# Kernel optimization log

Measured on AMD Instinct MI355X. Metric: run time of the kernel, lower is better.

Reference implementation:

```python
import jax, jax.numpy as jnp
import numpy as np

NR = 512      # num robots
NT = 1024     # num tasks
E = 500000    # num edges
D = 64        # robot_dim == task_dim (forced by torch.cat dim=0)
ED = 32       # edge_dim
GH = 128      # gnn_hidden
MH = 128      # mlp_hidden
SLOPE = 0.1   # LeakyReLU negative slope


def lrelu(x):
    return jnp.where(x >= 0, x, SLOPE * x)


def _linear(key, out_d, in_d):
    k1, k2 = jax.random.split(key)
    s = 1.0 / np.sqrt(in_d)
    W = jax.random.uniform(k1, (out_d, in_d), minval=-s, maxval=s, dtype=jnp.float32)
    b = jax.random.uniform(k2, (out_d,), minval=-s, maxval=s, dtype=jnp.float32)
    return W, b


def setup_inputs() -> dict:
    key = jax.random.key(0)
    ks = jax.random.split(key, 12)
    x_robot = jax.random.normal(ks[0], (NR, D), dtype=jnp.float32)
    x_task = jax.random.normal(ks[1], (NT, D), dtype=jnp.float32)
    edge_attr = jax.random.normal(ks[2], (E, ED), dtype=jnp.float32)
    src = jax.random.randint(ks[3], (E,), 0, NR)
    tgt = jax.random.randint(ks[4], (E,), 0, NT)
    edge_index = jnp.stack([src, tgt], axis=0).astype(jnp.int64)
    We1, be1 = _linear(ks[5], GH, 2 * D + ED)   # f_theta_e layer 1
    We2, be2 = _linear(ks[6], GH, GH)            # f_theta_e layer 2
    Wv1, bv1 = _linear(ks[7], GH, D + GH)        # f_theta_v layer 1
    Wv2, bv2 = _linear(ks[8], GH, GH)            # f_theta_v layer 2
    Wm1, bm1 = _linear(ks[9], MH, GH + D)        # task selector layer 1
    Wm2, bm2 = _linear(ks[10], 1, MH)            # task selector layer 2
    return {
        'x_robot': x_robot, 'x_task': x_task, 'edge_index': edge_index,
        'edge_attr': edge_attr,
        'We1': We1, 'be1': be1, 'We2': We2, 'be2': be2,
        'Wv1': Wv1, 'bv1': bv1, 'Wv2': Wv2, 'bv2': bv2,
        'Wm1': Wm1, 'bm1': bm1, 'Wm2': Wm2, 'bm2': bm2,
    }


def reference(x_robot, x_task, edge_index, edge_attr,
              We1, be1, We2, be2, Wv1, bv1, Wv2, bv2, Wm1, bm1, Wm2, bm2):
    n_robot = x_robot.shape[0]
    x = jnp.concatenate([x_robot, x_task], axis=0)          # [NR+NT, D]
    src = edge_index[0]                                      # robot indices
    tgt = edge_index[1] + n_robot                            # shifted task indices
    # PyG default flow='source_to_target': x_i = x[target], x_j = x[source],
    # messages are scatter-added at target slots (the task slots here).
    msg_in = jnp.concatenate([x[tgt], x[src], edge_attr], axis=1)  # [E, 2D+ED]
    m = lrelu(msg_in @ We1.T + be1) @ We2.T + be2            # [E, GH]
    agg = jax.ops.segment_sum(m, tgt, num_segments=n_robot + x_task.shape[0])
    robot_msgs = agg[:n_robot]                               # all zeros (faithful to source)
    upd_in = jnp.concatenate([robot_msgs, x_robot], axis=1)  # [NR, GH+D]
    h = lrelu(upd_in @ Wv1.T + bv1) @ Wv2.T + bv2            # [NR, GH]
    # Pairwise MLP on concat([h_i, task_j]) without materializing the concat:
    # split Wm1 columns into the robot-hidden and task parts.
    hr = h @ Wm1[:, :GH].T                                   # [NR, MH]
    ht = x_task @ Wm1[:, GH:].T                              # [NT, MH]
    hid = lrelu(hr[:, None, :] + ht[None, :, :] + bm1)       # [NR, NT, MH]
    scores = jnp.einsum('nmh,h->nm', hid, Wm2[0]) + bm2[0]   # [NR, NT]
    return jax.nn.softmax(scores, axis=1)
```

## Files before the change

kernel.cpp:

```cpp
#include <hip/hip_runtime.h>

#define NRB 512
#define NTK 1024
#define DD  64
#define GHH 128



__global__ __launch_bounds__(256) void prep_kernel(
    const float* __restrict__ xr, const float* __restrict__ xt,
    const float* __restrict__ Wv1, const float* __restrict__ bv1,
    const float* __restrict__ Wv2, const float* __restrict__ bv2,
    const float* __restrict__ Wm1, const float* __restrict__ bm1,
    const float* __restrict__ Wm2, const float* __restrict__ bm2,
    float* __restrict__ HR, float* __restrict__ HTBt4,
    float* __restrict__ av, float* __restrict__ cv, float* __restrict__ wbv)
{
    const int t = threadIdx.x;
    const int b = blockIdx.x;
    const int i = t & 127;
    const int g = t >> 7;

    __shared__ float lds_w[128 * 132];
    __shared__ float xs[8 * 64];
    __shared__ float sA[4 * 132];
    __shared__ float sB[4 * 132];
    __shared__ float sT[8 * 132];
    __shared__ float sR[8 * 132];

    float4* Lw = reinterpret_cast<float4*>(lds_w);

    if (b < 128) {
        const int r0 = b * 4;
        xs[t] = xr[r0 * DD + t];

        {
            const float4* W = reinterpret_cast<const float4*>(Wv1);
            #pragma unroll
            for (int j = 0; j < 8; ++j) {
                const int e = t + 256 * j;
                const int row = e >> 4, c4 = e & 15;
                Lw[row * 33 + c4] = W[row * 48 + 32 + c4];
            }
        }
        __syncthreads();

        {
            float a0 = bv1[i], a1 = a0;
            const float4* w4 = Lw + i * 33;
            const float4* x0 = reinterpret_cast<const float4*>(xs + (2*g)*64);
            const float4* x1 = reinterpret_cast<const float4*>(xs + (2*g+1)*64);
            #pragma unroll
            for (int k = 0; k < 16; ++k) {
                const float4 w = w4[k];
                const float4 p = x0[k];
                const float4 q = x1[k];
                a0 = fmaf(w.x, p.x, a0); a1 = fmaf(w.x, q.x, a1);
                a0 = fmaf(w.y, p.y, a0); a1 = fmaf(w.y, q.y, a1);
                a0 = fmaf(w.z, p.z, a0); a1 = fmaf(w.z, q.z, a1);
                a0 = fmaf(w.w, p.w, a0); a1 = fmaf(w.w, q.w, a1);
            }
            sA[(2*g)*132 + i]   = (a0 >= 0.f) ? a0 : 0.1f * a0;
            sA[(2*g+1)*132 + i] = (a1 >= 0.f) ? a1 : 0.1f * a1;
        }
        __syncthreads();

        {
            const float4* W = reinterpret_cast<const float4*>(Wv2);
            #pragma unroll
            for (int j = 0; j < 16; ++j) {
                const int e = t + 256 * j;
                const int row = e >> 5, c4 = e & 31;
                Lw[row * 33 + c4] = W[row * 32 + c4];
            }
        }
        __syncthreads();

        {
            float a0 = bv2[i], a1 = a0;
            const float4* w4 = Lw + i * 33;
            const float4* h0 = reinterpret_cast<const float4*>(sA + (2*g)*132);
            const float4* h1 = reinterpret_cast<const float4*>(sA + (2*g+1)*132);
            #pragma unroll 8
            for (int k = 0; k < 32; ++k) {
                const float4 w = w4[k];
                const float4 p = h0[k];
                const float4 q = h1[k];
                a0 = fmaf(w.x, p.x, a0); a1 = fmaf(w.x, q.x, a1);
                a0 = fmaf(w.y, p.y, a0); a1 = fmaf(w.y, q.y, a1);
                a0 = fmaf(w.z, p.z, a0); a1 = fmaf(w.z, q.z, a1);
                a0 = fmaf(w.w, p.w, a0); a1 = fmaf(w.w, q.w, a1);
            }
            sB[(2*g)*132 + i]   = a0;
            sB[(2*g+1)*132 + i] = a1;
        }
        __syncthreads();

        {
            const float4* W = reinterpret_cast<const float4*>(Wm1);
            #pragma unroll
            for (int j = 0; j < 16; ++j) {
                const int e = t + 256 * j;
                const int row = e >> 5, c4 = e & 31;
                Lw[row * 33 + c4] = W[row * 48 + c4];
            }
        }
        __syncthreads();

        {
            const float wm2 = Wm2[i];
            float a0 = 0.f, a1 = 0.f;
            const float4* w4 = Lw + i * 33;
            const float4* h0 = reinterpret_cast<const float4*>(sB + (2*g)*132);
            const float4* h1 = reinterpret_cast<const float4*>(sB + (2*g+1)*132);
            #pragma unroll 8
            for (int k = 0; k < 32; ++k) {
                const float4 w = w4[k];
                const float4 p = h0[k];
                const float4 q = h1[k];
                a0 = fmaf(w.x, p.x, a0); a1 = fmaf(w.x, q.x, a1);
                a0 = fmaf(w.y, p.y, a0); a1 = fmaf(w.y, q.y, a1);
                a0 = fmaf(w.z, p.z, a0); a1 = fmaf(w.z, q.z, a1);
                a0 = fmaf(w.w, p.w, a0); a1 = fmaf(w.w, q.w, a1);
            }
            HR[(r0 + 2*g) * GHH + i]     = a0;
            HR[(r0 + 2*g + 1) * GHH + i] = a1;
            sR[(2*g)*132 + i]   = wm2 * a0;
            sR[(2*g+1)*132 + i] = wm2 * a1;
        }
        __syncthreads();

        {
            const int row = t >> 6, c = t & 63;
            float s = sR[row*132 + c] + sR[row*132 + c + 64];
            #pragma unroll
            for (int off = 32; off >= 1; off >>= 1)
                s += __shfl_xor(s, off, 64);
            if (c == 0) av[r0 + row] = 0.55f * s;
        }
    } else {
        const int t0 = (b - 128) * 8;
        xs[t]       = xt[t0 * DD + t];
        xs[256 + t] = xt[t0 * DD + 256 + t];

        {
            const float4* W = reinterpret_cast<const float4*>(Wm1);
            #pragma unroll
            for (int j = 0; j < 8; ++j) {
                const int e = t + 256 * j;
                const int row = e >> 4, c4 = e & 15;
                Lw[row * 33 + c4] = W[row * 48 + 32 + c4];
            }
        }
        __syncthreads();

        {
            const float bb  = bm1[i];
            const float wm2 = Wm2[i];
            float a0 = bb, a1 = bb, a2 = bb, a3 = bb;
            const float4* w4 = Lw + i * 33;
            const float4* x0 = reinterpret_cast<const float4*>(xs + (4*g)*64);
            const float4* x1 = reinterpret_cast<const float4*>(xs + (4*g+1)*64);
            const float4* x2 = reinterpret_cast<const float4*>(xs + (4*g+2)*64);
            const float4* x3 = reinterpret_cast<const float4*>(xs + (4*g+3)*64);
            #pragma unroll
            for (int k = 0; k < 16; ++k) {
                const float4 w = w4[k];
                const float4 p0 = x0[k], p1 = x1[k], p2 = x2[k], p3 = x3[k];
                a0 = fmaf(w.x, p0.x, a0); a1 = fmaf(w.x, p1.x, a1);
                a2 = fmaf(w.x, p2.x, a2); a3 = fmaf(w.x, p3.x, a3);
                a0 = fmaf(w.y, p0.y, a0); a1 = fmaf(w.y, p1.y, a1);
                a2 = fmaf(w.y, p2.y, a2); a3 = fmaf(w.y, p3.y, a3);
                a0 = fmaf(w.z, p0.z, a0); a1 = fmaf(w.z, p1.z, a1);
                a2 = fmaf(w.z, p2.z, a2); a3 = fmaf(w.z, p3.z, a3);
                a0 = fmaf(w.w, p0.w, a0); a1 = fmaf(w.w, p1.w, a1);
                a2 = fmaf(w.w, p2.w, a2); a3 = fmaf(w.w, p3.w, a3);
            }
            sT[(4*g)*132 + i]   = a0;  sR[(4*g)*132 + i]   = wm2 * a0;
            sT[(4*g+1)*132 + i] = a1;  sR[(4*g+1)*132 + i] = wm2 * a1;
            sT[(4*g+2)*132 + i] = a2;  sR[(4*g+2)*132 + i] = wm2 * a2;
            sT[(4*g+3)*132 + i] = a3;  sR[(4*g+3)*132 + i] = wm2 * a3;
        }
        __syncthreads();

        {
            const int h4 = t >> 3, tk = t & 7;
            float4 v;
            v.x = sT[tk*132 + 4*h4 + 0];
            v.y = sT[tk*132 + 4*h4 + 1];
            v.z = sT[tk*132 + 4*h4 + 2];
            v.w = sT[tk*132 + 4*h4 + 3];
            reinterpret_cast<float4*>(HTBt4)[h4 * NTK + t0 + tk] = v;
        }

        {
            const int row = t >> 5, c = t & 31;
            float s = sR[row*132 + c]      + sR[row*132 + c + 32]
                    + sR[row*132 + c + 64] + sR[row*132 + c + 96];
            #pragma unroll
            for (int off = 16; off >= 1; off >>= 1)
                s += __shfl_xor(s, off, 32);
            if (c == 0) cv[t0 + row] = 0.55f * s + bm2[0];
        }
        if (b == 128 && t < GHH) wbv[t] = 0.45f * Wm2[t];
    }
}

__global__ __launch_bounds__(1024) void score_softmax_kernel(
    const float* __restrict__ HR, const float* __restrict__ HTBt4,
    const float* __restrict__ av, const float* __restrict__ cv,
    const float* __restrict__ wbv, float* __restrict__ out)
{
    const int b   = blockIdx.x;
    const int tid = threadIdx.x;
    const int n0  = b * 2;

    const float4* tb  = reinterpret_cast<const float4*>(HTBt4) + tid;
    const float4* hrA = reinterpret_cast<const float4*>(HR + n0 * GHH);
    const float4* hrB = reinterpret_cast<const float4*>(HR + (n0 + 1) * GHH);
    const float4* wb4 = reinterpret_cast<const float4*>(wbv);

    float acc0 = 0.f, acc1 = 0.f;

    #pragma unroll 4
    for (int h4 = 0; h4 < 32; ++h4) {
        const float4 v  = tb[h4 << 10];
        const float4 w  = wb4[h4];
        const float4 r0 = hrA[h4];
        const float4 r1 = hrB[h4];
        acc0 = fmaf(w.x, fabsf(r0.x + v.x), acc0);
        acc1 = fmaf(w.x, fabsf(r1.x + v.x), acc1);
        acc0 = fmaf(w.y, fabsf(r0.y + v.y), acc0);
        acc1 = fmaf(w.y, fabsf(r1.y + v.y), acc1);
        acc0 = fmaf(w.z, fabsf(r0.z + v.z), acc0);
        acc1 = fmaf(w.z, fabsf(r1.z + v.z), acc1);
        acc0 = fmaf(w.w, fabsf(r0.w + v.w), acc0);
        acc1 = fmaf(w.w, fabsf(r1.w + v.w), acc1);
    }

    const float cm = cv[tid];
    float sc[2];
    sc[0] = acc0 + av[n0]     + cm;
    sc[1] = acc1 + av[n0 + 1] + cm;

    __shared__ float rmax[2][16], rsum[2][16];
    const int wid = tid >> 6, lane = tid & 63;

    #pragma unroll
    for (int n = 0; n < 2; ++n) {
        float mx = sc[n];
        #pragma unroll
        for (int off = 32; off >= 1; off >>= 1)
            mx = fmaxf(mx, __shfl_xor(mx, off, 64));
        if (lane == 0) rmax[n][wid] = mx;
    }
    __syncthreads();

    float ex[2];
    #pragma unroll
    for (int n = 0; n < 2; ++n) {
        float mx = rmax[n][0];
        #pragma unroll
        for (int k = 1; k < 16; ++k) mx = fmaxf(mx, rmax[n][k]);
        float e = expf(sc[n] - mx);
        ex[n] = e;
        float s = e;
        #pragma unroll
        for (int off = 32; off >= 1; off >>= 1) s += __shfl_xor(s, off, 64);
        if (lane == 0) rsum[n][wid] = s;
    }
    __syncthreads();

    #pragma unroll
    for (int n = 0; n < 2; ++n) {
        float s = rsum[n][0];
        #pragma unroll
        for (int k = 1; k < 16; ++k) s += rsum[n][k];
        out[(n0 + n) * NTK + tid] = ex[n] * (1.0f / s);
    }
}

extern "C" void kernel_launch(void* const* d_in, const int* in_sizes, int n_in,
                              void* d_out, int out_size, void* d_ws, size_t ws_size,
                              hipStream_t stream)
{
    const float* xr  = (const float*)d_in[0];
    const float* xt  = (const float*)d_in[1];
    const float* Wv1 = (const float*)d_in[8];
    const float* bv1 = (const float*)d_in[9];
    const float* Wv2 = (const float*)d_in[10];
    const float* bv2 = (const float*)d_in[11];
    const float* Wm1 = (const float*)d_in[12];
    const float* bm1 = (const float*)d_in[13];
    const float* Wm2 = (const float*)d_in[14];
    const float* bm2 = (const float*)d_in[15];

    float* ws    = (float*)d_ws;
    float* HR    = ws;
    float* HTBt4 = ws + 65536;
    float* av    = ws + 196608;
    float* cv    = ws + 197120;
    float* wbv   = ws + 198144;
    float* out   = (float*)d_out;

    hipLaunchKernelGGL(prep_kernel, dim3(256), dim3(256), 0, stream,
                       xr, xt, Wv1, bv1, Wv2, bv2, Wm1, bm1, Wm2, bm2,
                       HR, HTBt4, av, cv, wbv);
    hipLaunchKernelGGL(score_softmax_kernel, dim3(256), dim3(1024), 0, stream,
                       HR, HTBt4, av, cv, wbv, out);
}
```

Measured before the change: 22.53 us.

## Fuse robot-side MLP into score/softmax kernel, keep task prep separate

Moves the robot hidden-state chain (Wv1, Wv2, Wm1 robot part, and the av term) out of the prep kernel and into the score/softmax kernel, where each block computes its two robots' HR rows in shared memory. The prep kernel now handles only task-side work, with half as many blocks. This removes the HR/av/wbv global round trip. In exchange, each 1024-thread score block reloads three 128x128 weight matrices into LDS, runs three serial matvecs on only 256 active threads, and needs about 70KB of LDS, which may limit occupancy.

```diff
diff --git a/kernel.cpp b/kernel.cpp
--- a/kernel.cpp
+++ b/kernel.cpp
@@ -7,14 +7,11 @@
 
 
 
-__global__ __launch_bounds__(256) void prep_kernel(
-    const float* __restrict__ xr, const float* __restrict__ xt,
-    const float* __restrict__ Wv1, const float* __restrict__ bv1,
-    const float* __restrict__ Wv2, const float* __restrict__ bv2,
+__global__ __launch_bounds__(256) void task_prep_kernel(
+    const float* __restrict__ xt,
     const float* __restrict__ Wm1, const float* __restrict__ bm1,
     const float* __restrict__ Wm2, const float* __restrict__ bm2,
-    float* __restrict__ HR, float* __restrict__ HTBt4,
-    float* __restrict__ av, float* __restrict__ cv, float* __restrict__ wbv)
+    float* __restrict__ HTBt4, float* __restrict__ cv)
 {
     const int t = threadIdx.x;
     const int b = blockIdx.x;
@@ -23,202 +20,206 @@
 
     __shared__ float lds_w[128 * 132];
     __shared__ float xs[8 * 64];
-    __shared__ float sA[4 * 132];
-    __shared__ float sB[4 * 132];
     __shared__ float sT[8 * 132];
     __shared__ float sR[8 * 132];
 
     float4* Lw = reinterpret_cast<float4*>(lds_w);
 
-    if (b < 128) {
-        const int r0 = b * 4;
-        xs[t] = xr[r0 * DD + t];
-
-        {
-            const float4* W = reinterpret_cast<const float4*>(Wv1);
-            #pragma unroll
-            for (int j = 0; j < 8; ++j) {
-                const int e = t + 256 * j;
-                const int row = e >> 4, c4 = e & 15;
-                Lw[row * 33 + c4] = W[row * 48 + 32 + c4];
-            }
-        }
-        __syncthreads();
-
-        {
-            float a0 = bv1[i], a1 = a0;
-            const float4* w4 = Lw + i * 33;
-            const float4* x0 = reinterpret_cast<const float4*>(xs + (2*g)*64);
-            const float4* x1 = reinterpret_cast<const float4*>(xs + (2*g+1)*64);
-            #pragma unroll
-            for (int k = 0; k < 16; ++k) {
-                const float4 w = w4[k];
-                const float4 p = x0[k];
-                const float4 q = x1[k];
-                a0 = fmaf(w.x, p.x, a0); a1 = fmaf(w.x, q.x, a1);
-                a0 = fmaf(w.y, p.y, a0); a1 = fmaf(w.y, q.y, a1);
-                a0 = fmaf(w.z, p.z, a0); a1 = fmaf(w.z, q.z, a1);
-                a0 = fmaf(w.w, p.w, a0); a1 = fmaf(w.w, q.w, a1);
-            }
-            sA[(2*g)*132 + i]   = (a0 >= 0.f) ? a0 : 0.1f * a0;
-            sA[(2*g+1)*132 + i] = (a1 >= 0.f) ? a1 : 0.1f * a1;
-        }
-        __syncthreads();
-
-        {
-            const float4* W = reinterpret_cast<const float4*>(Wv2);
-            #pragma unroll
-            for (int j = 0; j < 16; ++j) {
-                const int e = t + 256 * j;
-                const int row = e >> 5, c4 = e & 31;
-                Lw[row * 33 + c4] = W[row * 32 + c4];
-            }
-        }
-        __syncthreads();
-
-        {
-            float a0 = bv2[i], a1 = a0;
-            const float4* w4 = Lw + i * 33;
-            const float4* h0 = reinterpret_cast<const float4*>(sA + (2*g)*132);
-            const float4* h1 = reinterpret_cast<const float4*>(sA + (2*g+1)*132);
-            #pragma unroll 8
-            for (int k = 0; k < 32; ++k) {
-                const float4 w = w4[k];
-                const float4 p = h0[k];
-                const float4 q = h1[k];
-                a0 = fmaf(w.x, p.x, a0); a1 = fmaf(w.x, q.x, a1);
-                a0 = fmaf(w.y, p.y, a0); a1 = fmaf(w.y, q.y, a1);
-                a0 = fmaf(w.z, p.z, a0); a1 = fmaf(w.z, q.z, a1);
-                a0 = fmaf(w.w, p.w, a0); a1 = fmaf(w.w, q.w, a1);
-            }
-            sB[(2*g)*132 + i]   = a0;
-            sB[(2*g+1)*132 + i] = a1;
-        }
-        __syncthreads();
-
-        {
-            const float4* W = reinterpret_cast<const float4*>(Wm1);
-            #pragma unroll
-            for (int j = 0; j < 16; ++j) {
-                const int e = t + 256 * j;
-                const int row = e >> 5, c4 = e & 31;
-                Lw[row * 33 + c4] = W[row * 48 + c4];
-            }
-        }
-        __syncthreads();
-
-        {
-            const float wm2 = Wm2[i];
-            float a0 = 0.f, a1 = 0.f;
-            const float4* w4 = Lw + i * 33;
-            const float4* h0 = reinterpret_cast<const float4*>(sB + (2*g)*132);
-            const float4* h1 = reinterpret_cast<const float4*>(sB + (2*g+1)*132);
-            #pragma unroll 8
-            for (int k = 0; k < 32; ++k) {
-                const float4 w = w4[k];
-                const float4 p = h0[k];
-                const float4 q = h1[k];
-                a0 = fmaf(w.x, p.x, a0); a1 = fmaf(w.x, q.x, a1);
-                a0 = fmaf(w.y, p.y, a0); a1 = fmaf(w.y, q.y, a1);
-                a0 = fmaf(w.z, p.z, a0); a1 = fmaf(w.z, q.z, a1);
-                a0 = fmaf(w.w, p.w, a0); a1 = fmaf(w.w, q.w, a1);
-            }
-            HR[(r0 + 2*g) * GHH + i]     = a0;
-            HR[(r0 + 2*g + 1) * GHH + i] = a1;
-            sR[(2*g)*132 + i]   = wm2 * a0;
-            sR[(2*g+1)*132 + i] = wm2 * a1;
-        }
-        __syncthreads();
-
-        {
-            const int row = t >> 6, c = t & 63;
-            float s = sR[row*132 + c] + sR[row*132 + c + 64];
-            #pragma unroll
-            for (int off = 32; off >= 1; off >>= 1)
-                s += __shfl_xor(s, off, 64);
-            if (c == 0) av[r0 + row] = 0.55f * s;
-        }
-    } else {
-        const int t0 = (b - 128) * 8;
-        xs[t]       = xt[t0 * DD + t];
-        xs[256 + t] = xt[t0 * DD + 256 + t];
-
-        {
-            const float4* W = reinterpret_cast<const float4*>(Wm1);
-            #pragma unroll
-            for (int j = 0; j < 8; ++j) {
-                const int e = t + 256 * j;
-                const int row = e >> 4, c4 = e & 15;
-                Lw[row * 33 + c4] = W[row * 48 + 32 + c4];
-            }
-        }
-        __syncthreads();
-
-        {
-            const float bb  = bm1[i];
-            const float wm2 = Wm2[i];
-            float a0 = bb, a1 = bb, a2 = bb, a3 = bb;
-            const float4* w4 = Lw + i * 33;
-            const float4* x0 = reinterpret_cast<const float4*>(xs + (4*g)*64);
-            const float4* x1 = reinterpret_cast<const float4*>(xs + (4*g+1)*64);
-            const float4* x2 = reinterpret_cast<const float4*>(xs + (4*g+2)*64);
-            const float4* x3 = reinterpret_cast<const float4*>(xs + (4*g+3)*64);
-            #pragma unroll
-            for (int k = 0; k < 16; ++k) {
-                const float4 w = w4[k];
-                const float4 p0 = x0[k], p1 = x1[k], p2 = x2[k], p3 = x3[k];
-                a0 = fmaf(w.x, p0.x, a0); a1 = fmaf(w.x, p1.x, a1);
-                a2 = fmaf(w.x, p2.x, a2); a3 = fmaf(w.x, p3.x, a3);
-                a0 = fmaf(w.y, p0.y, a0); a1 = fmaf(w.y, p1.y, a1);
-                a2 = fmaf(w.y, p2.y, a2); a3 = fmaf(w.y, p3.y, a3);
-                a0 = fmaf(w.z, p0.z, a0); a1 = fmaf(w.z, p1.z, a1);
-                a2 = fmaf(w.z, p2.z, a2); a3 = fmaf(w.z, p3.z, a3);
-                a0 = fmaf(w.w, p0.w, a0); a1 = fmaf(w.w, p1.w, a1);
-                a2 = fmaf(w.w, p2.w, a2); a3 = fmaf(w.w, p3.w, a3);
-            }
-            sT[(4*g)*132 + i]   = a0;  sR[(4*g)*132 + i]   = wm2 * a0;
-            sT[(4*g+1)*132 + i] = a1;  sR[(4*g+1)*132 + i] = wm2 * a1;
-            sT[(4*g+2)*132 + i] = a2;  sR[(4*g+2)*132 + i] = wm2 * a2;
-            sT[(4*g+3)*132 + i] = a3;  sR[(4*g+3)*132 + i] = wm2 * a3;
-        }
-        __syncthreads();
-
-        {
-            const int h4 = t >> 3, tk = t & 7;
-            float4 v;
-            v.x = sT[tk*132 + 4*h4 + 0];
-            v.y = sT[tk*132 + 4*h4 + 1];
-            v.z = sT[tk*132 + 4*h4 + 2];
-            v.w = sT[tk*132 + 4*h4 + 3];
-            reinterpret_cast<float4*>(HTBt4)[h4 * NTK + t0 + tk] = v;
-        }
-
-        {
-            const int row = t >> 5, c = t & 31;
-            float s = sR[row*132 + c]      + sR[row*132 + c + 32]
-                    + sR[row*132 + c + 64] + sR[row*132 + c + 96];
-            #pragma unroll
-            for (int off = 16; off >= 1; off >>= 1)
-                s += __shfl_xor(s, off, 32);
-            if (c == 0) cv[t0 + row] = 0.55f * s + bm2[0];
-        }
-        if (b == 128 && t < GHH) wbv[t] = 0.45f * Wm2[t];
+    const int t0 = b * 8;
+    xs[t]       = xt[t0 * DD + t];
+    xs[256 + t] = xt[t0 * DD + 256 + t];
+
+    {
+        const float4* W = reinterpret_cast<const float4*>(Wm1);
+        #pragma unroll
+        for (int j = 0; j < 8; ++j) {
+            const int e = t + 256 * j;
+            const int row = e >> 4, c4 = e & 15;
+            Lw[row * 33 + c4] = W[row * 48 + 32 + c4];
+        }
+    }
+    __syncthreads();
+
+    {
+        const float bb  = bm1[i];
+        const float wm2 = Wm2[i];
+        float a0 = bb, a1 = bb, a2 = bb, a3 = bb;
+        const float4* w4 = Lw + i * 33;
+        const float4* x0 = reinterpret_cast<const float4*>(xs + (4*g)*64);
+        const float4* x1 = reinterpret_cast<const float4*>(xs + (4*g+1)*64);
+        const float4* x2 = reinterpret_cast<const float4*>(xs + (4*g+2)*64);
+        const float4* x3 = reinterpret_cast<const float4*>(xs + (4*g+3)*64);
+        #pragma unroll
+        for (int k = 0; k < 16; ++k) {
+            const float4 w = w4[k];
+            const float4 p0 = x0[k], p1 = x1[k], p2 = x2[k], p3 = x3[k];
+            a0 = fmaf(w.x, p0.x, a0); a1 = fmaf(w.x, p1.x, a1);
+            a2 = fmaf(w.x, p2.x, a2); a3 = fmaf(w.x, p3.x, a3);
+            a0 = fmaf(w.y, p0.y, a0); a1 = fmaf(w.y, p1.y, a1);
+            a2 = fmaf(w.y, p2.y, a2); a3 = fmaf(w.y, p3.y, a3);
+            a0 = fmaf(w.z, p0.z, a0); a1 = fmaf(w.z, p1.z, a1);
+            a2 = fmaf(w.z, p2.z, a2); a3 = fmaf(w.z, p3.z, a3);
+            a0 = fmaf(w.w, p0.w, a0); a1 = fmaf(w.w, p1.w, a1);
+            a2 = fmaf(w.w, p2.w, a2); a3 = fmaf(w.w, p3.w, a3);
+        }
+        sT[(4*g)*132 + i]   = a0;  sR[(4*g)*132 + i]   = wm2 * a0;
+        sT[(4*g+1)*132 + i] = a1;  sR[(4*g+1)*132 + i] = wm2 * a1;
+        sT[(4*g+2)*132 + i] = a2;  sR[(4*g+2)*132 + i] = wm2 * a2;
+        sT[(4*g+3)*132 + i] = a3;  sR[(4*g+3)*132 + i] = wm2 * a3;
+    }
+    __syncthreads();
+
+    {
+        const int h4 = t >> 3, tk = t & 7;
+        float4 v;
+        v.x = sT[tk*132 + 4*h4 + 0];
+        v.y = sT[tk*132 + 4*h4 + 1];
+        v.z = sT[tk*132 + 4*h4 + 2];
+        v.w = sT[tk*132 + 4*h4 + 3];
+        reinterpret_cast<float4*>(HTBt4)[h4 * NTK + t0 + tk] = v;
+    }
+
+    {
+        const int row = t >> 5, c = t & 31;
+        float s = sR[row*132 + c]      + sR[row*132 + c + 32]
+                + sR[row*132 + c + 64] + sR[row*132 + c + 96];
+        #pragma unroll
+        for (int off = 16; off >= 1; off >>= 1)
+            s += __shfl_xor(s, off, 32);
+        if (c == 0) cv[t0 + row] = 0.55f * s + bm2[0];
     }
 }
 
-__global__ __launch_bounds__(1024) void score_softmax_kernel(
-    const float* __restrict__ HR, const float* __restrict__ HTBt4,
-    const float* __restrict__ av, const float* __restrict__ cv,
-    const float* __restrict__ wbv, float* __restrict__ out)
+__global__ __launch_bounds__(1024) void robot_score_softmax_kernel(
+    const float* __restrict__ xr,
+    const float* __restrict__ Wv1, const float* __restrict__ bv1,
+    const float* __restrict__ Wv2, const float* __restrict__ bv2,
+    const float* __restrict__ Wm1, const float* __restrict__ Wm2,
+    const float* __restrict__ HTBt4, const float* __restrict__ cv,
+    float* __restrict__ out)
 {
     const int b   = blockIdx.x;
     const int tid = threadIdx.x;
     const int n0  = b * 2;
 
+    __shared__ float lds_w[128 * 132];
+    __shared__ float xs[2 * 64];
+    __shared__ float sA[2 * 132];
+    __shared__ float sB[2 * 132];
+    __shared__ float sR[2 * 132];
+    __shared__ float s_hr[2 * 128];
+    __shared__ float s_wb[128];
+    __shared__ float s_av[2];
+
+    float4* Lw = reinterpret_cast<float4*>(lds_w);
+
+    const float cm = cv[tid];
+
+    if (tid < 128) xs[tid] = xr[n0 * DD + tid];
+
+    {
+        const float4* W = reinterpret_cast<const float4*>(Wv1);
+        #pragma unroll
+        for (int j = 0; j < 2; ++j) {
+            const int e = tid + 1024 * j;
+            const int row = e >> 4, c4 = e & 15;
+            Lw[row * 33 + c4] = W[row * 48 + 32 + c4];
+        }
+    }
+    __syncthreads();
+
+    if (tid < 256) {
+        const int i = tid & 127, r = tid >> 7;
+        float acc = bv1[i];
+        const float4* w4 = Lw + i * 33;
+        const float4* x4 = reinterpret_cast<const float4*>(xs + r * 64);
+        #pragma unroll
+        for (int k = 0; k < 16; ++k) {
+            const float4 w = w4[k];
+            const float4 p = x4[k];
+            acc = fmaf(w.x, p.x, acc);
+            acc = fmaf(w.y, p.y, acc);
+            acc = fmaf(w.z, p.z, acc);
+            acc = fmaf(w.w, p.w, acc);
+        }
+        sA[r*132 + i] = (acc >= 0.f) ? acc : 0.1f * acc;
+    }
+    __syncthreads();
+
+    {
+        const float4* W = reinterpret_cast<const float4*>(Wv2);
+        #pragma unroll
+        for (int j = 0; j < 4; ++j) {
+            const int e = tid + 1024 * j;
+            const int row = e >> 5, c4 = e & 31;
+            Lw[row * 33 + c4] = W[row * 32 + c4];
+        }
+    }
+    __syncthreads();
+
+    if (tid < 256) {
+        const int i = tid & 127, r = tid >> 7;
+        float acc = bv2[i];
+        const float4* w4 = Lw + i * 33;
+        const float4* h4 = reinterpret_cast<const float4*>(sA + r * 132);
+        #pragma unroll 8
+        for (int k = 0; k < 32; ++k) {
+            const float4 w = w4[k];
+            const float4 p = h4[k];
+            acc = fmaf(w.x, p.x, acc);
+            acc = fmaf(w.y, p.y, acc);
+            acc = fmaf(w.z, p.z, acc);
+            acc = fmaf(w.w, p.w, acc);
+        }
+        sB[r*132 + i] = acc;
+    }
+    __syncthreads();
+
+    {
+        const float4* W = reinterpret_cast<const float4*>(Wm1);
+        #pragma unroll
+        for (int j = 0; j < 4; ++j) {
+            const int e = tid + 1024 * j;
+            const int row = e >> 5, c4 = e & 31;
+            Lw[row * 33 + c4] = W[row * 48 + c4];
+        }
+        if (tid < 128) s_wb[tid] = 0.45f * Wm2[tid];
+    }
+    __syncthreads();
+
+    if (tid < 256) {
+        const int i = tid & 127, r = tid >> 7;
+        float acc = 0.f;
+        const float4* w4 = Lw + i * 33;
+        const float4* h4 = reinterpret_cast<const float4*>(sB + r * 132);
+        #pragma unroll 8
+        for (int k = 0; k < 32; ++k) {
+            const float4 w = w4[k];
+            const float4 p = h4[k];
+            acc = fmaf(w.x, p.x, acc);
+            acc = fmaf(w.y, p.y, acc);
+            acc = fmaf(w.z, p.z, acc);
+            acc = fmaf(w.w, p.w, acc);
+        }
+        s_hr[r*128 + i] = acc;
+        sR[r*132 + i]   = Wm2[i] * acc;
+    }
+    __syncthreads();
+
+    if (tid < 128) {
+        const int w = tid >> 6, l = tid & 63;
+        float s = sR[w*132 + l] + sR[w*132 + l + 64];
+        #pragma unroll
+        for (int off = 32; off >= 1; off >>= 1)
+            s += __shfl_xor(s, off, 64);
+        if (l == 0) s_av[w] = 0.55f * s;
+    }
+    __syncthreads();
+
     const float4* tb  = reinterpret_cast<const float4*>(HTBt4) + tid;
-    const float4* hrA = reinterpret_cast<const float4*>(HR + n0 * GHH);
-    const float4* hrB = reinterpret_cast<const float4*>(HR + (n0 + 1) * GHH);
-    const float4* wb4 = reinterpret_cast<const float4*>(wbv);
+    const float4* hrA = reinterpret_cast<const float4*>(s_hr);
+    const float4* hrB = reinterpret_cast<const float4*>(s_hr + 128);
+    const float4* wb4 = reinterpret_cast<const float4*>(s_wb);
 
     float acc0 = 0.f, acc1 = 0.f;
 
@@ -238,10 +239,9 @@
         acc1 = fmaf(w.w, fabsf(r1.w + v.w), acc1);
     }
 
-    const float cm = cv[tid];
     float sc[2];
-    sc[0] = acc0 + av[n0]     + cm;
-    sc[1] = acc1 + av[n0 + 1] + cm;
+    sc[0] = acc0 + s_av[0] + cm;
+    sc[1] = acc1 + s_av[1] + cm;
 
     __shared__ float rmax[2][16], rsum[2][16];
     const int wid = tid >> 6, lane = tid & 63;
@@ -296,16 +296,12 @@
     const float* bm2 = (const float*)d_in[15];
 
     float* ws    = (float*)d_ws;
-    float* HR    = ws;
-    float* HTBt4 = ws + 65536;
-    float* av    = ws + 196608;
-    float* cv    = ws + 197120;
-    float* wbv   = ws + 198144;
+    float* HTBt4 = ws;
+    float* cv    = ws + 131072;
     float* out   = (float*)d_out;
 
-    hipLaunchKernelGGL(prep_kernel, dim3(256), dim3(256), 0, stream,
-                       xr, xt, Wv1, bv1, Wv2, bv2, Wm1, bm1, Wm2, bm2,
-                       HR, HTBt4, av, cv, wbv);
-    hipLaunchKernelGGL(score_softmax_kernel, dim3(256), dim3(1024), 0, stream,
-                       HR, HTBt4, av, cv, wbv, out);
+    hipLaunchKernelGGL(task_prep_kernel, dim3(128), dim3(256), 0, stream,
+                       xt, Wm1, bm1, Wm2, bm2, HTBt4, cv);
+    hipLaunchKernelGGL(robot_score_softmax_kernel, dim3(256), dim3(1024), 0, stream,
+                       xr, Wv1, bv1, Wv2, bv2, Wm1, Wm2, HTBt4, cv, out);
 }
```

New measurement: 24.42 us. 1.08x slower.

## Double rows per block in prep and score kernels, staging HR in shared memory

Applied to the files above, without the earlier changes.

The prep kernel now handles 8 robots or 16 tasks per block, halving the grid to 128 blocks, so each staged weight matrix is reused across twice as many rows. The score/softmax kernel processes 4 robot rows per block instead of 2, with the HR rows and the weight vector staged in LDS, so each loaded HTBt4 tile serves four accumulators. Both changes cut redundant global weight loads. In exchange there are fewer blocks than the GPU's CUs, which lowers parallelism and may hurt latency hiding, and registers per thread go up.

```diff
diff --git a/kernel.cpp b/kernel.cpp
--- a/kernel.cpp
+++ b/kernel.cpp
@@ -22,17 +22,20 @@
     const int g = t >> 7;
 
     __shared__ float lds_w[128 * 132];
-    __shared__ float xs[8 * 64];
-    __shared__ float sA[4 * 132];
-    __shared__ float sB[4 * 132];
-    __shared__ float sT[8 * 132];
-    __shared__ float sR[8 * 132];
+    __shared__ float xs[16 * 64];
+    __shared__ float sU[16 * 132];
+    __shared__ float sV[16 * 132];
 
     float4* Lw = reinterpret_cast<float4*>(lds_w);
 
-    if (b < 128) {
-        const int r0 = b * 4;
-        xs[t] = xr[r0 * DD + t];
+    if (b < 64) {
+        const int r0 = b * 8;
+        xs[t]       = xr[r0 * DD + t];
+        xs[256 + t] = xr[r0 * DD + 256 + t];
+
+        float* sA = sU;
+        float* sB = sV;
+        float* sR = sU + 8 * 132;
 
         {
             const float4* W = reinterpret_cast<const float4*>(Wv1);
@@ -46,117 +49,7 @@
         __syncthreads();
 
         {
-            float a0 = bv1[i], a1 = a0;
-            const float4* w4 = Lw + i * 33;
-            const float4* x0 = reinterpret_cast<const float4*>(xs + (2*g)*64);
-            const float4* x1 = reinterpret_cast<const float4*>(xs + (2*g+1)*64);
-            #pragma unroll
-            for (int k = 0; k < 16; ++k) {
-                const float4 w = w4[k];
-                const float4 p = x0[k];
-                const float4 q = x1[k];
-                a0 = fmaf(w.x, p.x, a0); a1 = fmaf(w.x, q.x, a1);
-                a0 = fmaf(w.y, p.y, a0); a1 = fmaf(w.y, q.y, a1);
-                a0 = fmaf(w.z, p.z, a0); a1 = fmaf(w.z, q.z, a1);
-                a0 = fmaf(w.w, p.w, a0); a1 = fmaf(w.w, q.w, a1);
-            }
-            sA[(2*g)*132 + i]   = (a0 >= 0.f) ? a0 : 0.1f * a0;
-            sA[(2*g+1)*132 + i] = (a1 >= 0.f) ? a1 : 0.1f * a1;
-        }
-        __syncthreads();
-
-        {
-            const float4* W = reinterpret_cast<const float4*>(Wv2);
-            #pragma unroll
-            for (int j = 0; j < 16; ++j) {
-                const int e = t + 256 * j;
-                const int row = e >> 5, c4 = e & 31;
-                Lw[row * 33 + c4] = W[row * 32 + c4];
-            }
-        }
-        __syncthreads();
-
-        {
-            float a0 = bv2[i], a1 = a0;
-            const float4* w4 = Lw + i * 33;
-            const float4* h0 = reinterpret_cast<const float4*>(sA + (2*g)*132);
-            const float4* h1 = reinterpret_cast<const float4*>(sA + (2*g+1)*132);
-            #pragma unroll 8
-            for (int k = 0; k < 32; ++k) {
-                const float4 w = w4[k];
-                const float4 p = h0[k];
-                const float4 q = h1[k];
-                a0 = fmaf(w.x, p.x, a0); a1 = fmaf(w.x, q.x, a1);
-                a0 = fmaf(w.y, p.y, a0); a1 = fmaf(w.y, q.y, a1);
-                a0 = fmaf(w.z, p.z, a0); a1 = fmaf(w.z, q.z, a1);
-                a0 = fmaf(w.w, p.w, a0); a1 = fmaf(w.w, q.w, a1);
-            }
-            sB[(2*g)*132 + i]   = a0;
-            sB[(2*g+1)*132 + i] = a1;
-        }
-        __syncthreads();
-
-        {
-            const float4* W = reinterpret_cast<const float4*>(Wm1);
-            #pragma unroll
-            for (int j = 0; j < 16; ++j) {
-                const int e = t + 256 * j;
-                const int row = e >> 5, c4 = e & 31;
-                Lw[row * 33 + c4] = W[row * 48 + c4];
-            }
-        }
-        __syncthreads();
-
-        {
-            const float wm2 = Wm2[i];
-            float a0 = 0.f, a1 = 0.f;
-            const float4* w4 = Lw + i * 33;
-            const float4* h0 = reinterpret_cast<const float4*>(sB + (2*g)*132);
-            const float4* h1 = reinterpret_cast<const float4*>(sB + (2*g+1)*132);
-            #pragma unroll 8
-            for (int k = 0; k < 32; ++k) {
-                const float4 w = w4[k];
-                const float4 p = h0[k];
-                const float4 q = h1[k];
-                a0 = fmaf(w.x, p.x, a0); a1 = fmaf(w.x, q.x, a1);
-                a0 = fmaf(w.y, p.y, a0); a1 = fmaf(w.y, q.y, a1);
-                a0 = fmaf(w.z, p.z, a0); a1 = fmaf(w.z, q.z, a1);
-                a0 = fmaf(w.w, p.w, a0); a1 = fmaf(w.w, q.w, a1);
-            }
-            HR[(r0 + 2*g) * GHH + i]     = a0;
-            HR[(r0 + 2*g + 1) * GHH + i] = a1;
-            sR[(2*g)*132 + i]   = wm2 * a0;
-            sR[(2*g+1)*132 + i] = wm2 * a1;
-        }
-        __syncthreads();
-
-        {
-            const int row = t >> 6, c = t & 63;
-            float s = sR[row*132 + c] + sR[row*132 + c + 64];
-            #pragma unroll
-            for (int off = 32; off >= 1; off >>= 1)
-                s += __shfl_xor(s, off, 64);
-            if (c == 0) av[r0 + row] = 0.55f * s;
-        }
-    } else {
-        const int t0 = (b - 128) * 8;
-        xs[t]       = xt[t0 * DD + t];
-        xs[256 + t] = xt[t0 * DD + 256 + t];
-
-        {
-            const float4* W = reinterpret_cast<const float4*>(Wm1);
-            #pragma unroll
-            for (int j = 0; j < 8; ++j) {
-                const int e = t + 256 * j;
-                const int row = e >> 4, c4 = e & 15;
-                Lw[row * 33 + c4] = W[row * 48 + 32 + c4];
-            }
-        }
-        __syncthreads();
-
-        {
-            const float bb  = bm1[i];
-            const float wm2 = Wm2[i];
+            const float bb = bv1[i];
             float a0 = bb, a1 = bb, a2 = bb, a3 = bb;
             const float4* w4 = Lw + i * 33;
             const float4* x0 = reinterpret_cast<const float4*>(xs + (4*g)*64);
@@ -176,15 +69,183 @@
                 a0 = fmaf(w.w, p0.w, a0); a1 = fmaf(w.w, p1.w, a1);
                 a2 = fmaf(w.w, p2.w, a2); a3 = fmaf(w.w, p3.w, a3);
             }
-            sT[(4*g)*132 + i]   = a0;  sR[(4*g)*132 + i]   = wm2 * a0;
-            sT[(4*g+1)*132 + i] = a1;  sR[(4*g+1)*132 + i] = wm2 * a1;
-            sT[(4*g+2)*132 + i] = a2;  sR[(4*g+2)*132 + i] = wm2 * a2;
-            sT[(4*g+3)*132 + i] = a3;  sR[(4*g+3)*132 + i] = wm2 * a3;
-        }
-        __syncthreads();
-
-        {
-            const int h4 = t >> 3, tk = t & 7;
+            sA[(4*g)*132 + i]   = (a0 >= 0.f) ? a0 : 0.1f * a0;
+            sA[(4*g+1)*132 + i] = (a1 >= 0.f) ? a1 : 0.1f * a1;
+            sA[(4*g+2)*132 + i] = (a2 >= 0.f) ? a2 : 0.1f * a2;
+            sA[(4*g+3)*132 + i] = (a3 >= 0.f) ? a3 : 0.1f * a3;
+        }
+        __syncthreads();
+
+        {
+            const float4* W = reinterpret_cast<const float4*>(Wv2);
+            #pragma unroll
+            for (int j = 0; j < 16; ++j) {
+                const int e = t + 256 * j;
+                const int row = e >> 5, c4 = e & 31;
+                Lw[row * 33 + c4] = W[row * 32 + c4];
+            }
+        }
+        __syncthreads();
+
+        {
+            const float bb = bv2[i];
+            float a0 = bb, a1 = bb, a2 = bb, a3 = bb;
+            const float4* w4 = Lw + i * 33;
+            const float4* h0 = reinterpret_cast<const float4*>(sA + (4*g)*132);
+            const float4* h1 = reinterpret_cast<const float4*>(sA + (4*g+1)*132);
+            const float4* h2 = reinterpret_cast<const float4*>(sA + (4*g+2)*132);
+            const float4* h3 = reinterpret_cast<const float4*>(sA + (4*g+3)*132);
+            #pragma unroll 8
+            for (int k = 0; k < 32; ++k) {
+                const float4 w = w4[k];
+                const float4 p0 = h0[k], p1 = h1[k], p2 = h2[k], p3 = h3[k];
+                a0 = fmaf(w.x, p0.x, a0); a1 = fmaf(w.x, p1.x, a1);
+                a2 = fmaf(w.x, p2.x, a2); a3 = fmaf(w.x, p3.x, a3);
+                a0 = fmaf(w.y, p0.y, a0); a1 = fmaf(w.y, p1.y, a1);
+                a2 = fmaf(w.y, p2.y, a2); a3 = fmaf(w.y, p3.y, a3);
+                a0 = fmaf(w.z, p0.z, a0); a1 = fmaf(w.z, p1.z, a1);
+                a2 = fmaf(w.z, p2.z, a2); a3 = fmaf(w.z, p3.z, a3);
+                a0 = fmaf(w.w, p0.w, a0); a1 = fmaf(w.w, p1.w, a1);
+                a2 = fmaf(w.w, p2.w, a2); a3 = fmaf(w.w, p3.w, a3);
+            }
+            sB[(4*g)*132 + i]   = a0;
+            sB[(4*g+1)*132 + i] = a1;
+            sB[(4*g+2)*132 + i] = a2;
+            sB[(4*g+3)*132 + i] = a3;
+        }
+        __syncthreads();
+
+        {
+            const float4* W = reinterpret_cast<const float4*>(Wm1);
+            #pragma unroll
+            for (int j = 0; j < 16; ++j) {
+                const int e = t + 256 * j;
+                const int row = e >> 5, c4 = e & 31;
+                Lw[row * 33 + c4] = W[row * 48 + c4];
+            }
+        }
+        __syncthreads();
+
+        {
+            const float wm2 = Wm2[i];
+            float a0 = 0.f, a1 = 0.f, a2 = 0.f, a3 = 0.f;
+            const float4* w4 = Lw + i * 33;
+            const float4* h0 = reinterpret_cast<const float4*>(sB + (4*g)*132);
+            const float4* h1 = reinterpret_cast<const float4*>(sB + (4*g+1)*132);
+            const float4* h2 = reinterpret_cast<const float4*>(sB + (4*g+2)*132);
+            const float4* h3 = reinterpret_cast<const float4*>(sB + (4*g+3)*132);
+            #pragma unroll 8
+            for (int k = 0; k < 32; ++k) {
+                const float4 w = w4[k];
+                const float4 p0 = h0[k], p1 = h1[k], p2 = h2[k], p3 = h3[k];
+                a0 = fmaf(w.x, p0.x, a0); a1 = fmaf(w.x, p1.x, a1);
+                a2 = fmaf(w.x, p2.x, a2); a3 = fmaf(w.x, p3.x, a3);
+                a0 = fmaf(w.y, p0.y, a0); a1 = fmaf(w.y, p1.y, a1);
+                a2 = fmaf(w.y, p2.y, a2); a3 = fmaf(w.y, p3.y, a3);
+                a0 = fmaf(w.z, p0.z, a0); a1 = fmaf(w.z, p1.z, a1);
+                a2 = fmaf(w.z, p2.z, a2); a3 = fmaf(w.z, p3.z, a3);
+                a0 = fmaf(w.w, p0.w, a0); a1 = fmaf(w.w, p1.w, a1);
+                a2 = fmaf(w.w, p2.w, a2); a3 = fmaf(w.w, p3.w, a3);
+            }
+            HR[(r0 + 4*g)     * GHH + i] = a0;
+            HR[(r0 + 4*g + 1) * GHH + i] = a1;
+            HR[(r0 + 4*g + 2) * GHH + i] = a2;
+            HR[(r0 + 4*g + 3) * GHH + i] = a3;
+            sR[(4*g)*132 + i]   = wm2 * a0;
+            sR[(4*g+1)*132 + i] = wm2 * a1;
+            sR[(4*g+2)*132 + i] = wm2 * a2;
+            sR[(4*g+3)*132 + i] = wm2 * a3;
+        }
+        __syncthreads();
+
+        {
+            const int row = t >> 5, c = t & 31;
+            float s = sR[row*132 + c]      + sR[row*132 + c + 32]
+                    + sR[row*132 + c + 64] + sR[row*132 + c + 96];
+            #pragma unroll
+            for (int off = 16; off >= 1; off >>= 1)
+                s += __shfl_xor(s, off, 32);
+            if (c == 0) av[r0 + row] = 0.55f * s;
+        }
+    } else {
+        const int t0 = (b - 64) * 16;
+        xs[t]       = xt[t0 * DD + t];
+        xs[256 + t] = xt[t0 * DD + 256 + t];
+        xs[512 + t] = xt[t0 * DD + 512 + t];
+        xs[768 + t] = xt[t0 * DD + 768 + t];
+
+        float* sT = sU;
+        float* sR = sV;
+
+        {
+            const float4* W = reinterpret_cast<const float4*>(Wm1);
+            #pragma unroll
+            for (int j = 0; j < 8; ++j) {
+                const int e = t + 256 * j;
+                const int row = e >> 4, c4 = e & 15;
+                Lw[row * 33 + c4] = W[row * 48 + 32 + c4];
+            }
+        }
+        __syncthreads();
+
+        {
+            const float bb  = bm1[i];
+            const float wm2 = Wm2[i];
+            float a0 = bb, a1 = bb, a2 = bb, a3 = bb;
+            float a4 = bb, a5 = bb, a6 = bb, a7 = bb;
+            const float4* w4 = Lw + i * 33;
+            const float4* x0 = reinterpret_cast<const float4*>(xs + (8*g)*64);
+            const float4* x1 = reinterpret_cast<const float4*>(xs + (8*g+1)*64);
+            const float4* x2 = reinterpret_cast<const float4*>(xs + (8*g+2)*64);
+            const float4* x3 = reinterpret_cast<const float4*>(xs + (8*g+3)*64);
+            const float4* x4 = reinterpret_cast<const float4*>(xs + (8*g+4)*64);
+            const float4* x5 = reinterpret_cast<const float4*>(xs + (8*g+5)*64);
+            const float4* x6 = reinterpret_cast<const float4*>(xs + (8*g+6)*64);
+            const float4* x7 = reinterpret_cast<const float4*>(xs + (8*g+7)*64);
+            #pragma unroll
+            for (int k = 0; k < 16; ++k) {
+                const float4 w = w4[k];
+                float4 p;
+                p = x0[k];
+                a0 = fmaf(w.x, p.x, a0); a0 = fmaf(w.y, p.y, a0);
+                a0 = fmaf(w.z, p.z, a0); a0 = fmaf(w.w, p.w, a0);
+                p = x1[k];
+                a1 = fmaf(w.x, p.x, a1); a1 = fmaf(w.y, p.y, a1);
+                a1 = fmaf(w.z, p.z, a1); a1 = fmaf(w.w, p.w, a1);
+                p = x2[k];
+                a2 = fmaf(w.x, p.x, a2); a2 = fmaf(w.y, p.y, a2);
+                a2 = fmaf(w.z, p.z, a2); a2 = fmaf(w.w, p.w, a2);
+                p = x3[k];
+                a3 = fmaf(w.x, p.x, a3); a3 = fmaf(w.y, p.y, a3);
+                a3 = fmaf(w.z, p.z, a3); a3 = fmaf(w.w, p.w, a3);
+                p = x4[k];
+                a4 = fmaf(w.x, p.x, a4); a4 = fmaf(w.y, p.y, a4);
+                a4 = fmaf(w.z, p.z, a4); a4 = fmaf(w.w, p.w, a4);
+                p = x5[k];
+                a5 = fmaf(w.x, p.x, a5); a5 = fmaf(w.y, p.y, a5);
+                a5 = fmaf(w.z, p.z, a5); a5 = fmaf(w.w, p.w, a5);
+                p = x6[k];
+                a6 = fmaf(w.x, p.x, a6); a6 = fmaf(w.y, p.y, a6);
+                a6 = fmaf(w.z, p.z, a6); a6 = fmaf(w.w, p.w, a6);
+                p = x7[k];
+                a7 = fmaf(w.x, p.x, a7); a7 = fmaf(w.y, p.y, a7);
+                a7 = fmaf(w.z, p.z, a7); a7 = fmaf(w.w, p.w, a7);
+            }
+            sT[(8*g)*132 + i]   = a0;  sR[(8*g)*132 + i]   = wm2 * a0;
+            sT[(8*g+1)*132 + i] = a1;  sR[(8*g+1)*132 + i] = wm2 * a1;
+            sT[(8*g+2)*132 + i] = a2;  sR[(8*g+2)*132 + i] = wm2 * a2;
+            sT[(8*g+3)*132 + i] = a3;  sR[(8*g+3)*132 + i] = wm2 * a3;
+            sT[(8*g+4)*132 + i] = a4;  sR[(8*g+4)*132 + i] = wm2 * a4;
+            sT[(8*g+5)*132 + i] = a5;  sR[(8*g+5)*132 + i] = wm2 * a5;
+            sT[(8*g+6)*132 + i] = a6;  sR[(8*g+6)*132 + i] = wm2 * a6;
+            sT[(8*g+7)*132 + i] = a7;  sR[(8*g+7)*132 + i] = wm2 * a7;
+        }
+        __syncthreads();
+
+        #pragma unroll
+        for (int j = 0; j < 2; ++j) {
+            const int e  = t + 256 * j;
+            const int h4 = e >> 4, tk = e & 15;
             float4 v;
             v.x = sT[tk*132 + 4*h4 + 0];
             v.y = sT[tk*132 + 4*h4 + 1];
@@ -194,15 +255,16 @@
         }
 
         {
-            const int row = t >> 5, c = t & 31;
-            float s = sR[row*132 + c]      + sR[row*132 + c + 32]
-                    + sR[row*132 + c + 64] + sR[row*132 + c + 96];
-            #pragma unroll
-            for (int off = 16; off >= 1; off >>= 1)
-                s += __shfl_xor(s, off, 32);
+            const int row = t >> 4, c = t & 15;
+            float s = 0.f;
+            #pragma unroll
+            for (int j = 0; j < 8; ++j) s += sR[row*132 + c + 16*j];
+            #pragma unroll
+            for (int off = 8; off >= 1; off >>= 1)
+                s += __shfl_xor(s, off, 16);
             if (c == 0) cv[t0 + row] = 0.55f * s + bm2[0];
         }
-        if (b == 128 && t < GHH) wbv[t] = 0.45f * Wm2[t];
+        if (b == 64 && t < GHH) wbv[t] = 0.45f * Wm2[t];
     }
 }
 
@@ -213,41 +275,58 @@
 {
     const int b   = blockIdx.x;
     const int tid = threadIdx.x;
-    const int n0  = b * 2;
+    const int n0  = b * 4;
+
+    __shared__ float s_hr[4 * GHH];
+    __shared__ float s_wb[GHH];
+    if (tid < 512)      s_hr[tid]       = HR[n0 * GHH + tid];
+    else if (tid < 640) s_wb[tid - 512] = wbv[tid - 512];
+    const float cm = cv[tid];
+    __syncthreads();
 
     const float4* tb  = reinterpret_cast<const float4*>(HTBt4) + tid;
-    const float4* hrA = reinterpret_cast<const float4*>(HR + n0 * GHH);
-    const float4* hrB = reinterpret_cast<const float4*>(HR + (n0 + 1) * GHH);
-    const float4* wb4 = reinterpret_cast<const float4*>(wbv);
-
-    float acc0 = 0.f, acc1 = 0.f;
+    const float4* hr4 = reinterpret_cast<const float4*>(s_hr);
+    const float4* wb4 = reinterpret_cast<const float4*>(s_wb);
+
+    float acc0 = 0.f, acc1 = 0.f, acc2 = 0.f, acc3 = 0.f;
 
     #pragma unroll 4
     for (int h4 = 0; h4 < 32; ++h4) {
         const float4 v  = tb[h4 << 10];
         const float4 w  = wb4[h4];
-        const float4 r0 = hrA[h4];
-        const float4 r1 = hrB[h4];
+        const float4 r0 = hr4[h4];
+        const float4 r1 = hr4[32 + h4];
+        const float4 r2 = hr4[64 + h4];
+        const float4 r3 = hr4[96 + h4];
         acc0 = fmaf(w.x, fabsf(r0.x + v.x), acc0);
         acc1 = fmaf(w.x, fabsf(r1.x + v.x), acc1);
+        acc2 = fmaf(w.x, fabsf(r2.x + v.x), acc2);
+        acc3 = fmaf(w.x, fabsf(r3.x + v.x), acc3);
         acc0 = fmaf(w.y, fabsf(r0.y + v.y), acc0);
         acc1 = fmaf(w.y, fabsf(r1.y + v.y), acc1);
+        acc2 = fmaf(w.y, fabsf(r2.y + v.y), acc2);
+        acc3 = fmaf(w.y, fabsf(r3.y + v.y), acc3);
         acc0 = fmaf(w.z, fabsf(r0.z + v.z), acc0);
         acc1 = fmaf(w.z, fabsf(r1.z + v.z), acc1);
+        acc2 = fmaf(w.z, fabsf(r2.z + v.z), acc2);
+        acc3 = fmaf(w.z, fabsf(r3.z + v.z), acc3);
         acc0 = fmaf(w.w, fabsf(r0.w + v.w), acc0);
         acc1 = fmaf(w.w, fabsf(r1.w + v.w), acc1);
-    }
-
-    const float cm = cv[tid];
-    float sc[2];
+        acc2 = fmaf(w.w, fabsf(r2.w + v.w), acc2);
+        acc3 = fmaf(w.w, fabsf(r3.w + v.w), acc3);
+    }
+
+    float sc[4];
     sc[0] = acc0 + av[n0]     + cm;
     sc[1] = acc1 + av[n0 + 1] + cm;
-
-    __shared__ float rmax[2][16], rsum[2][16];
+    sc[2] = acc2 + av[n0 + 2] + cm;
+    sc[3] = acc3 + av[n0 + 3] + cm;
+
+    __shared__ float rmax[4][16], rsum[4][16];
     const int wid = tid >> 6, lane = tid & 63;
 
     #pragma unroll
-    for (int n = 0; n < 2; ++n) {
+    for (int n = 0; n < 4; ++n) {
         float mx = sc[n];
         #pragma unroll
         for (int off = 32; off >= 1; off >>= 1)
@@ -256,9 +335,9 @@
     }
     __syncthreads();
 
-    float ex[2];
+    float ex[4];
     #pragma unroll
-    for (int n = 0; n < 2; ++n) {
+    for (int n = 0; n < 4; ++n) {
         float mx = rmax[n][0];
         #pragma unroll
         for (int k = 1; k < 16; ++k) mx = fmaxf(mx, rmax[n][k]);
@@ -272,7 +351,7 @@
     __syncthreads();
 
     #pragma unroll
-    for (int n = 0; n < 2; ++n) {
+    for (int n = 0; n < 4; ++n) {
         float s = rsum[n][0];
         #pragma unroll
         for (int k = 1; k < 16; ++k) s += rsum[n][k];
@@ -303,9 +382,9 @@
     float* wbv   = ws + 198144;
     float* out   = (float*)d_out;
 
-    hipLaunchKernelGGL(prep_kernel, dim3(256), dim3(256), 0, stream,
+    hipLaunchKernelGGL(prep_kernel, dim3(128), dim3(256), 0, stream,
                        xr, xt, Wv1, bv1, Wv2, bv2, Wm1, bm1, Wm2, bm2,
                        HR, HTBt4, av, cv, wbv);
-    hipLaunchKernelGGL(score_softmax_kernel, dim3(256), dim3(1024), 0, stream,
+    hipLaunchKernelGGL(score_softmax_kernel, dim3(128), dim3(1024), 0, stream,
                        HR, HTBt4, av, cv, wbv, out);
 }
```

Measured after the change: 34.04 us. +51.1%, slower.
